# Kernel optimization log

Measured on AMD Instinct MI355X. Metric: run time of the kernel, lower is better.

Reference implementation:

```python
import jax, jax.numpy as jnp
import numpy as np

N_NODES = 50000
N_EDGES = 800000
IN_DIM = 128
HID = 64
HEADS = 4
OUT_DIM = 128
NEG_SLOPE = 0.2


def setup_inputs() -> dict:
    key = jax.random.key(0)
    ks = jax.random.split(key, 11)
    x = jax.random.normal(ks[0], (N_NODES, IN_DIM), dtype=jnp.float32)
    edge_index = jax.random.randint(ks[1], (2, N_EDGES), 0, N_NODES, dtype=jnp.int64)
    s1 = 1.0 / np.sqrt(IN_DIM)
    s2 = 1.0 / np.sqrt(HEADS * HID)
    W1 = jax.random.normal(ks[2], (IN_DIM, HEADS * HID), dtype=jnp.float32) * s1
    a_src1 = jax.random.normal(ks[3], (HEADS, HID), dtype=jnp.float32) * s2
    a_dst1 = jax.random.normal(ks[4], (HEADS, HID), dtype=jnp.float32) * s2
    b1 = jnp.zeros((HEADS * HID,), dtype=jnp.float32)
    W2 = jax.random.normal(ks[5], (HEADS * HID, OUT_DIM), dtype=jnp.float32) * s2
    a_src2 = jax.random.normal(ks[6], (1, OUT_DIM), dtype=jnp.float32) * 0.1
    a_dst2 = jax.random.normal(ks[7], (1, OUT_DIM), dtype=jnp.float32) * 0.1
    b2 = jnp.zeros((OUT_DIM,), dtype=jnp.float32)
    return {"x": x, "edge_index": edge_index, "W1": W1, "a_src1": a_src1,
            "a_dst1": a_dst1, "b1": b1, "W2": W2, "a_src2": a_src2,
            "a_dst2": a_dst2, "b2": b2}


def _gat_conv(x, src, dst, W, a_src, a_dst, bias, heads, out_per_head, concat):
    n = x.shape[0]
    # linear projection per head: [N, H, F]
    h = (x @ W).reshape(n, heads, out_per_head)
    # per-node attention terms: [N, H]
    alpha_src = jnp.einsum('nhf,hf->nh', h, a_src)
    alpha_dst = jnp.einsum('nhf,hf->nh', h, a_dst)
    # edge logits with LeakyReLU: [E, H]
    e = jax.nn.leaky_relu(alpha_src[src] + alpha_dst[dst], NEG_SLOPE)
    # softmax over incoming edges of each destination node
    m = jax.ops.segment_max(e, dst, num_segments=n)  # [N, H]
    m = jnp.where(jnp.isfinite(m), m, 0.0)
    e = jnp.exp(e - m[dst])
    denom = jax.ops.segment_sum(e, dst, num_segments=n)  # [N, H]
    alpha = e / (denom[dst] + 1e-16)  # [E, H]
    # weighted scatter-aggregate of source messages
    out = jax.ops.segment_sum(h[src] * alpha[:, :, None], dst, num_segments=n)  # [N, H, F]
    if concat:
        out = out.reshape(n, heads * out_per_head)
    else:
        out = out.mean(axis=1)
    return out + bias


def reference(x, edge_index, W1, a_src1, a_dst1, b1, W2, a_src2, a_dst2, b2):
    n = x.shape[0]
    # PyG GATConv adds self-loops by default
    loops = jnp.arange(n, dtype=edge_index.dtype)
    src = jnp.concatenate([edge_index[0], loops])
    dst = jnp.concatenate([edge_index[1], loops])
    # dropout layers are identity in inference
    h = _gat_conv(x, src, dst, W1, a_src1, a_dst1, b1, HEADS, HID, True)
    h = jax.nn.elu(h)
    out = _gat_conv(h, src, dst, W2, a_src2, a_dst2, b2, 1, OUT_DIM, True)
    # F.normalize(p=2, dim=1)
    norm = jnp.linalg.norm(out, axis=1, keepdims=True)
    return out / jnp.maximum(norm, 1e-12)
```

## Files before the change

kernel.cpp:

```cpp
#include <hip/hip_runtime.h>
#include <hip/hip_fp16.h>
#include <math.h>

#define N_NODES 50000
#define N_EDGES 800000
#define ET (N_EDGES + N_NODES)
#define IN_DIM 128
#define HID 64
#define HEADS 4
#define C1 (HEADS * HID)
#define OUT_DIM 128
#define NEG_SLOPE 0.2f
#define MTILES 3125
#define G1GRP 782
#define SCAN_B 1024
#define NSCB 49
#define HB 64
#define EPB (N_EDGES / HB)
#define HQ 4
#define NQN (N_NODES / HQ)

typedef _Float16 h8 __attribute__((ext_vector_type(8)));
typedef float f4 __attribute__((ext_vector_type(4)));
typedef unsigned short u16;

__device__ __forceinline__ float leaky(float v) { return fmaxf(v, NEG_SLOPE * v); }
__device__ __forceinline__ float elu(float v) { return v > 0.0f ? v : expm1f(v); }

__device__ __forceinline__ void fma_mix8(float* acc, h8 v, float w) {
    union { h8 h; int i[4]; } u; u.h = v;
#pragma unroll
    for (int k = 0; k < 4; ++k) {
        asm("v_fma_mix_f32 %0, %1, %2, %0 op_sel:[0,0,0] op_sel_hi:[1,0,0]"
            : "+v"(acc[2 * k]) : "v"(u.i[k]), "v"(w));
        asm("v_fma_mix_f32 %0, %1, %2, %0 op_sel:[1,0,0] op_sel_hi:[1,0,0]"
            : "+v"(acc[2 * k + 1]) : "v"(u.i[k]), "v"(w));
    }
}

__global__ void transpose_w(const float* __restrict__ W1, const float* __restrict__ W2,
                            __half* __restrict__ w1t, __half* __restrict__ w2t) {
    int i = blockIdx.x * 256 + threadIdx.x;
    int k1 = i >> 8, n1 = i & 255;
    w1t[n1 * IN_DIM + k1] = __float2half(W1[i]);
    int k2 = i >> 7, n2 = i & 127;
    w2t[n2 * C1 + k2] = __float2half(W2[i]);
}

__global__ __launch_bounds__(256) void gemm1_hist(
        const float* __restrict__ x, const __half* __restrict__ w1t,
        const float* __restrict__ aws, const float* __restrict__ awd,
        __half* __restrict__ hpm, float* __restrict__ as1m, float* __restrict__ ad1m,
        const int* __restrict__ dst, u16* __restrict__ cnt_mat,
        u16* __restrict__ lrank16) {
    __shared__ unsigned pk[NQN / 2];
    if (blockIdx.x < HB) {
        const int b = blockIdx.x, t = threadIdx.x;
        const int e0 = b * EPB;
#pragma unroll
        for (int qd = 0; qd < HQ; ++qd) {
            const int nbase = qd * NQN;
            for (int i = t; i < NQN / 2; i += 256) pk[i] = 0;
            __syncthreads();
            for (int k = t; k < EPB; k += 256) {
                int d = dst[e0 + k] - nbase;
                if ((unsigned)d < (unsigned)NQN) {
                    unsigned r = atomicAdd(&pk[d >> 1], (d & 1) ? 65536u : 1u);
                    lrank16[e0 + k] = (u16)((d & 1) ? (r >> 16) : (r & 0xffffu));
                }
            }
            __syncthreads();
            unsigned* crow = (unsigned*)(cnt_mat + (size_t)b * N_NODES) + qd * (NQN / 2);
            for (int i = t; i < NQN / 2; i += 256) crow[i] = pk[i];
            __syncthreads();
        }
        return;
    }
    const int tile = (blockIdx.x - HB) * 4 + (threadIdx.x >> 6);
    if (tile >= MTILES) return;
    const int lane = threadIdx.x & 63;
    const int m0 = tile * 16, lm = lane & 15, lq = lane >> 4;
    h8 afrag[4];
    const float4* xrow = (const float4*)(x + (size_t)(m0 + lm) * IN_DIM + lq * 8);
#pragma unroll
    for (int kt = 0; kt < 4; ++kt) {
        float4 a = xrow[kt * 8];
        float4 b = xrow[kt * 8 + 1];
        union { h8 v; __half2 p[4]; } u;
        u.p[0] = __floats2half2_rn(a.x, a.y);
        u.p[1] = __floats2half2_rn(a.z, a.w);
        u.p[2] = __floats2half2_rn(b.x, b.y);
        u.p[3] = __floats2half2_rn(b.z, b.w);
        afrag[kt] = u.v;
    }
    f4 acc[16];
#pragma unroll
    for (int nt = 0; nt < 16; ++nt) acc[nt] = (f4){0.f, 0.f, 0.f, 0.f};
#pragma unroll
    for (int nt = 0; nt < 16; ++nt) {
        const h8* brow = (const h8*)(w1t + (size_t)(nt * 16 + lm) * IN_DIM + lq * 8);
#pragma unroll
        for (int kt = 0; kt < 4; ++kt)
            acc[nt] = __builtin_amdgcn_mfma_f32_16x16x32_f16(afrag[kt], brow[kt * 4],
                                                             acc[nt], 0, 0, 0);
    }
    float sS[4][4] = {{0.f}}, sD[4][4] = {{0.f}};
#pragma unroll
    for (int nt = 0; nt < 16; ++nt) {
        int col = nt * 16 + lm;
        float wa = aws[col], wd = awd[col];
        int hd = nt >> 2;
        int pr = nt >> 3;
        int cip = col & 127;
#pragma unroll
        for (int r = 0; r < 4; ++r) {
            float v = acc[nt][r];
            hpm[((size_t)pr * N_NODES + (m0 + lq * 4 + r)) * 128 + cip] = __float2half(v);
            sS[hd][r] += v * wa;
            sD[hd][r] += v * wd;
        }
    }
#pragma unroll
    for (int o = 1; o < 16; o <<= 1) {
#pragma unroll
        for (int hd = 0; hd < 4; ++hd)
#pragma unroll
            for (int r = 0; r < 4; ++r) {
                sS[hd][r] += __shfl_xor(sS[hd][r], o);
                sD[hd][r] += __shfl_xor(sD[hd][r], o);
            }
    }
    if (lm == 0) {
        float2* asp = (float2*)as1m;
        float2* adp = (float2*)ad1m;
#pragma unroll
        for (int r = 0; r < 4; ++r) {
            int row = m0 + lq * 4 + r;
            asp[row]           = make_float2(sS[0][r], sS[1][r]);
            asp[N_NODES + row] = make_float2(sS[2][r], sS[3][r]);
            adp[row]           = make_float2(sD[0][r], sD[1][r]);
            adp[N_NODES + row] = make_float2(sD[2][r], sD[3][r]);
        }
    }
}

__global__ void scan_local(const u16* __restrict__ cnt_mat, u16* __restrict__ boff,
                           int* __restrict__ lscan, int* __restrict__ bsum) {
    __shared__ int wsum[16];
    const int t = threadIdx.x, lane = t & 63, wv = t >> 6;
    int idx = blockIdx.x * SCAN_B + t;
    int run = 0;
    if (idx < N_NODES) {
#pragma unroll 8
        for (int b = 0; b < HB; ++b) {
            u16 c = cnt_mat[(size_t)b * N_NODES + idx];
            boff[(size_t)b * N_NODES + idx] = (u16)run;
            run += c;
        }
    }
    int v = (idx < N_NODES) ? run + 1 : 0;
    int sc = v;
#pragma unroll
    for (int o = 1; o < 64; o <<= 1) {
        int u = __shfl_up(sc, o);
        if (lane >= o) sc += u;
    }
    if (lane == 63) wsum[wv] = sc;
    __syncthreads();
    if (t == 0) {
        int run2 = 0;
#pragma unroll
        for (int w = 0; w < 16; ++w) { int s = wsum[w]; wsum[w] = run2; run2 += s; }
        bsum[blockIdx.x] = run2;
    }
    __syncthreads();
    if (idx < N_NODES) lscan[idx] = sc + wsum[wv];
}

__global__ void scan_final(const int* __restrict__ lscan, const int* __restrict__ bsum,
                           int* __restrict__ rp) {
    __shared__ int base;
    if (threadIdx.x == 0) {
        int s = 0;
        for (int b = 0; b < blockIdx.x; ++b) s += bsum[b];
        base = s;
    }
    __syncthreads();
    int idx = blockIdx.x * SCAN_B + threadIdx.x;
    if (idx == 0) rp[0] = 0;
    if (idx >= N_NODES) return;
    rp[idx + 1] = lscan[idx] + base;
}

__global__ void scatter_plain(const int* __restrict__ src, const int* __restrict__ dst,
                              const u16* __restrict__ lrank16, const u16* __restrict__ boff,
                              const int* __restrict__ rp, u16* __restrict__ cs16) {
    const int tid = blockIdx.x * blockDim.x + threadIdx.x;
    if (tid < N_EDGES / 4) {
        const int b = tid / (EPB / 4);
        const u16* bo = boff + (size_t)b * N_NODES;
        int4 s4 = ((const int4*)src)[tid];
        int4 d4 = ((const int4*)dst)[tid];
        ushort4 r4 = ((const ushort4*)lrank16)[tid];
        cs16[rp[d4.x] + (int)bo[d4.x] + (int)r4.x] = (u16)s4.x;
        cs16[rp[d4.y] + (int)bo[d4.y] + (int)r4.y] = (u16)s4.y;
        cs16[rp[d4.z] + (int)bo[d4.z] + (int)r4.z] = (u16)s4.z;
        cs16[rp[d4.w] + (int)bo[d4.w] + (int)r4.w] = (u16)s4.w;
    } else {
        int d = tid - N_EDGES / 4;
        if (d < N_NODES) cs16[rp[d + 1] - 1] = (u16)d;
    }
}

__global__ __launch_bounds__(256) void gemm2_mfma(
        const __half* __restrict__ ah, const __half* __restrict__ w2t,
        const float* __restrict__ aws, const float* __restrict__ awd,
        __half* __restrict__ h, float* __restrict__ as2, float* __restrict__ ad2) {
    const int tile = blockIdx.x * 4 + (threadIdx.x >> 6);
    if (tile >= MTILES) return;
    const int lane = threadIdx.x & 63;
    const int m0 = tile * 16, lm = lane & 15, lq = lane >> 4;
    h8 afrag[8];
    const h8* arow = (const h8*)(ah + (size_t)(m0 + lm) * C1 + lq * 8);
#pragma unroll
    for (int kt = 0; kt < 8; ++kt) afrag[kt] = arow[kt * 4];
    f4 acc[8];
#pragma unroll
    for (int nt = 0; nt < 8; ++nt) acc[nt] = (f4){0.f, 0.f, 0.f, 0.f};
#pragma unroll
    for (int nt = 0; nt < 8; ++nt) {
        const h8* brow = (const h8*)(w2t + (size_t)(nt * 16 + lm) * C1 + lq * 8);
#pragma unroll
        for (int kt = 0; kt < 8; ++kt)
            acc[nt] = __builtin_amdgcn_mfma_f32_16x16x32_f16(afrag[kt], brow[kt * 4],
                                                             acc[nt], 0, 0, 0);
    }
    float sS[4] = {0.f, 0.f, 0.f, 0.f}, sD[4] = {0.f, 0.f, 0.f, 0.f};
#pragma unroll
    for (int nt = 0; nt < 8; ++nt) {
        int col = nt * 16 + lm;
        float wa = aws[col], wd = awd[col];
#pragma unroll
        for (int r = 0; r < 4; ++r) {
            float v = acc[nt][r];
            h[(size_t)(m0 + lq * 4 + r) * OUT_DIM + col] = __float2half(v);
            sS[r] += v * wa;
            sD[r] += v * wd;
        }
    }
#pragma unroll
    for (int o = 1; o < 16; o <<= 1) {
#pragma unroll
        for (int r = 0; r < 4; ++r) {
            sS[r] += __shfl_xor(sS[r], o);
            sD[r] += __shfl_xor(sD[r], o);
        }
    }
    if (lm == 0) {
#pragma unroll
        for (int r = 0; r < 4; ++r) {
            int row = m0 + lq * 4 + r;
            as2[row] = sS[r];
            ad2[row] = sD[r];
        }
    }
}

__global__ __launch_bounds__(256) void aggregate1_fused(
        const int* __restrict__ rp, const u16* __restrict__ cs16,
        const __half* __restrict__ hpm, const float* __restrict__ as1m,
        const float* __restrict__ ad1m, const float* __restrict__ b1,
        __half* __restrict__ out1h) {
    __shared__ int4 stg[8][32];
    const int pair = blockIdx.x & 1, g = blockIdx.x >> 1;
    const int hw = threadIdx.x >> 5, li = threadIdx.x & 31;
    const int d = g * 8 + hw;
    const int e0 = rp[d], deg = rp[d + 1] - e0;
    const float2* asb = (const float2*)as1m + (size_t)pair * N_NODES;
    const float2 adv = ((const float2*)ad1m)[(size_t)pair * N_NODES + d];
    const char* hb = (const char*)hpm + (size_t)pair * N_NODES * 256;
    const int es = li >> 4, fl = li & 15;
    const int hip = fl >> 3;
    const int lbyte = fl * 16;
    float acc[8] = {0.f, 0.f, 0.f, 0.f, 0.f, 0.f, 0.f, 0.f};
    float ds0 = 0.f, ds1 = 0.f;
    for (int c0 = 0; c0 < deg; c0 += 32) {
        const int clen = min(32, deg - c0);
        int idx = c0 + li;
        bool valid = idx < deg;
        int s = valid ? (int)cs16[e0 + idx] : 0;
        float2 av = asb[s];
        float x0 = valid ? __expf(leaky(av.x + adv.x)) : 0.f;
        float x1 = valid ? __expf(leaky(av.y + adv.y)) : 0.f;
        stg[hw][li] = make_int4(s << 8, __float_as_int(x0), __float_as_int(x1), 0);
        ds0 += x0; ds1 += x1;
        __builtin_amdgcn_wave_barrier();
        int j = 0;
        for (; j + 8 <= clen; j += 8) {
            int4 p0 = stg[hw][j + es];
            int4 p1 = stg[hw][j + 2 + es];
            int4 p2 = stg[hw][j + 4 + es];
            int4 p3 = stg[hw][j + 6 + es];
            h8 v0 = *(const h8*)(hb + p0.x + lbyte);
            h8 v1 = *(const h8*)(hb + p1.x + lbyte);
            h8 v2 = *(const h8*)(hb + p2.x + lbyte);
            h8 v3 = *(const h8*)(hb + p3.x + lbyte);
            fma_mix8(acc, v0, __int_as_float(hip ? p0.z : p0.y));
            fma_mix8(acc, v1, __int_as_float(hip ? p1.z : p1.y));
            fma_mix8(acc, v2, __int_as_float(hip ? p2.z : p2.y));
            fma_mix8(acc, v3, __int_as_float(hip ? p3.z : p3.y));
        }
        for (; j < clen; j += 2) {
            int4 p0 = stg[hw][j + es];
            h8 v0 = *(const h8*)(hb + p0.x + lbyte);
            fma_mix8(acc, v0, __int_as_float(hip ? p0.z : p0.y));
        }
        __builtin_amdgcn_wave_barrier();
    }
#pragma unroll
    for (int f = 0; f < 8; ++f) acc[f] += __shfl_xor(acc[f], 16);
#pragma unroll
    for (int o = 16; o > 0; o >>= 1) {
        ds0 += __shfl_xor(ds0, o);
        ds1 += __shfl_xor(ds1, o);
    }
    if (es == 0) {
        float den = hip ? ds1 : ds0;
        float inv = 1.0f / (den + 1e-16f);
        float4 bA = ((const float4*)b1)[pair * 32 + fl * 2];
        float4 bB = ((const float4*)b1)[pair * 32 + fl * 2 + 1];
        h8 o;
        o[0] = (_Float16)elu(acc[0] * inv + bA.x);
        o[1] = (_Float16)elu(acc[1] * inv + bA.y);
        o[2] = (_Float16)elu(acc[2] * inv + bA.z);
        o[3] = (_Float16)elu(acc[3] * inv + bA.w);
        o[4] = (_Float16)elu(acc[4] * inv + bB.x);
        o[5] = (_Float16)elu(acc[5] * inv + bB.y);
        o[6] = (_Float16)elu(acc[6] * inv + bB.z);
        o[7] = (_Float16)elu(acc[7] * inv + bB.w);
        *(h8*)((char*)out1h + (size_t)d * 512 + pair * 256 + lbyte) = o;
    }
}

__global__ __launch_bounds__(256) void aggregate2_fused(
        const int* __restrict__ rp, const u16* __restrict__ cs16,
        const __half* __restrict__ h2h, const float* __restrict__ as2,
        const float* __restrict__ ad2, const float* __restrict__ b2,
        float* __restrict__ out) {
    __shared__ int2 stg[8][32];
    const int hw = threadIdx.x >> 5, li = threadIdx.x & 31;
    const int d = blockIdx.x * 8 + hw;
    const int e0 = rp[d], deg = rp[d + 1] - e0;
    const float adv = ad2[d];
    const int q = li >> 4, lo = li & 15;
    const int lbyte = lo * 16;
    const char* hbase = (const char*)h2h;
    float acc[8] = {0.f, 0.f, 0.f, 0.f, 0.f, 0.f, 0.f, 0.f};
    float dsum = 0.f;
    for (int c0 = 0; c0 < deg; c0 += 32) {
        const int clen = min(32, deg - c0);
        int idx = c0 + li;
        bool valid = idx < deg;
        int s = valid ? (int)cs16[e0 + idx] : 0;
        float xv = valid ? __expf(leaky(as2[s] + adv)) : 0.f;
        stg[hw][li] = make_int2(s << 8, __float_as_int(xv));
        dsum += xv;
        __builtin_amdgcn_wave_barrier();
        int j = 0;
        for (; j + 8 <= clen; j += 8) {
            int2 p0 = stg[hw][j + q];
            int2 p1 = stg[hw][j + 2 + q];
            int2 p2 = stg[hw][j + 4 + q];
            int2 p3 = stg[hw][j + 6 + q];
            h8 v0 = *(const h8*)(hbase + p0.x + lbyte);
            h8 v1 = *(const h8*)(hbase + p1.x + lbyte);
            h8 v2 = *(const h8*)(hbase + p2.x + lbyte);
            h8 v3 = *(const h8*)(hbase + p3.x + lbyte);
            fma_mix8(acc, v0, __int_as_float(p0.y));
            fma_mix8(acc, v1, __int_as_float(p1.y));
            fma_mix8(acc, v2, __int_as_float(p2.y));
            fma_mix8(acc, v3, __int_as_float(p3.y));
        }
        for (; j < clen; j += 2) {
            int2 p0 = stg[hw][j + q];
            h8 v0 = *(const h8*)(hbase + p0.x + lbyte);
            fma_mix8(acc, v0, __int_as_float(p0.y));
        }
        __builtin_amdgcn_wave_barrier();
    }
#pragma unroll
    for (int f = 0; f < 8; ++f) acc[f] += __shfl_xor(acc[f], 16);
#pragma unroll
    for (int o = 16; o > 0; o >>= 1) dsum += __shfl_xor(dsum, o);
    if (q == 0) {
        float inv = 1.0f / (dsum + 1e-16f);
        float4 bA = ((const float4*)b2)[lo * 2];
        float4 bB = ((const float4*)b2)[lo * 2 + 1];
        float v0 = acc[0] * inv + bA.x, v1 = acc[1] * inv + bA.y;
        float v2 = acc[2] * inv + bA.z, v3 = acc[3] * inv + bA.w;
        float v4 = acc[4] * inv + bB.x, v5 = acc[5] * inv + bB.y;
        float v6 = acc[6] * inv + bB.z, v7 = acc[7] * inv + bB.w;
        float ss = v0 * v0 + v1 * v1 + v2 * v2 + v3 * v3 +
                   v4 * v4 + v5 * v5 + v6 * v6 + v7 * v7;
#pragma unroll
        for (int o = 1; o < 16; o <<= 1) ss += __shfl_xor(ss, o);
        float sc = 1.0f / fmaxf(sqrtf(ss), 1e-12f);
        float4* orow = (float4*)((char*)out + (size_t)d * 512 + lo * 32);
        orow[0] = make_float4(v0 * sc, v1 * sc, v2 * sc, v3 * sc);
        orow[1] = make_float4(v4 * sc, v5 * sc, v6 * sc, v7 * sc);
    }
}

extern "C" void kernel_launch(void* const* d_in, const int* in_sizes, int n_in,
                              void* d_out, int out_size, void* d_ws, size_t ws_size,
                              hipStream_t stream) {
    const float* x     = (const float*)d_in[0];
    const int*   edge  = (const int*)d_in[1];
    const int*   src   = edge;
    const int*   dst   = edge + N_EDGES;
    const float* W1    = (const float*)d_in[2];
    const float* aw_s1 = (const float*)d_in[3];
    const float* aw_d1 = (const float*)d_in[4];
    const float* b1    = (const float*)d_in[5];
    const float* W2    = (const float*)d_in[6];
    const float* aw_s2 = (const float*)d_in[7];
    const float* aw_d2 = (const float*)d_in[8];
    const float* b2    = (const float*)d_in[9];
    float* out = (float*)d_out;

    char* ws = (char*)d_ws;
    size_t off = 0;
    auto alloc = [&](size_t bytes) {
        void* p = ws + off;
        off += (bytes + 255) & ~(size_t)255;
        return p;
    };
    u16*    cs16    = (u16*)alloc((size_t)ET * 2);
    u16*    lrank16 = (u16*)alloc((size_t)N_EDGES * 2);
    u16*    cnt_mat = (u16*)alloc((size_t)HB * N_NODES * 2);
    u16*    boff    = (u16*)alloc((size_t)HB * N_NODES * 2);
    int*    rp      = (int*)alloc((size_t)(N_NODES + 1) * 4);
    int*    lscan   = (int*)alloc((size_t)NSCB * SCAN_B * 4);
    int*    bsum    = (int*)alloc((size_t)NSCB * 4);
    float*  as1     = (float*)alloc((size_t)N_NODES * HEADS * 4);
    float*  ad1     = (float*)alloc((size_t)N_NODES * HEADS * 4);
    float*  as2     = (float*)alloc((size_t)N_NODES * 4);
    float*  ad2     = (float*)alloc((size_t)N_NODES * 4);
    __half* w1t     = (__half*)alloc((size_t)IN_DIM * C1 * 2);
    __half* w2t     = (__half*)alloc((size_t)C1 * OUT_DIM * 2);
    __half* hpm     = (__half*)alloc((size_t)N_NODES * C1 * 2);
    __half* out1h   = (__half*)alloc((size_t)N_NODES * C1 * 2);
    __half* h2h     = hpm;
    (void)off;


    transpose_w<<<(IN_DIM * C1) / 256, 256, 0, stream>>>(W1, W2, w1t, w2t);

    gemm1_hist<<<HB + G1GRP, 256, 0, stream>>>(x, w1t, aw_s1, aw_d1, hpm, as1, ad1,
                                               dst, cnt_mat, lrank16);

    scan_local<<<NSCB, SCAN_B, 0, stream>>>(cnt_mat, boff, lscan, bsum);
    scan_final<<<NSCB, SCAN_B, 0, stream>>>(lscan, bsum, rp);
    scatter_plain<<<(N_EDGES / 4 + N_NODES + 255) / 256, 256, 0, stream>>>(
        src, dst, lrank16, boff, rp, cs16);

    aggregate1_fused<<<(N_NODES / 8) * 2, 256, 0, stream>>>(rp, cs16, hpm, as1, ad1, b1, out1h);

    gemm2_mfma<<<(MTILES + 3) / 4, 256, 0, stream>>>(out1h, w2t, aw_s2, aw_d2, h2h, as2, ad2);
    aggregate2_fused<<<N_NODES / 8, 256, 0, stream>>>(rp, cs16, h2h, as2, ad2, b2, out);
}
```

Before: 306.3 us.

## Split fused gemm1/histogram kernel into separate hist and GEMM launches

Splits the kernel that co-scheduled the edge histogram with the first projection GEMM into a standalone histogram kernel and a standalone MFMA GEMM launched after the scatter. The histogram now uses two node halves with a larger 50KB shared array instead of four quarters, and reads dst as int4 vectors. The intent is to stop the large LDS allocation from limiting occupancy of the GEMM blocks and to cut histogram passes. The cost is an extra launch and no more overlap between histogram and GEMM, and the 64 histogram blocks run on their own with little parallelism.

```diff
diff --git a/kernel.cpp b/kernel.cpp
--- a/kernel.cpp
+++ b/kernel.cpp
@@ -12,13 +12,10 @@
 #define OUT_DIM 128
 #define NEG_SLOPE 0.2f
 #define MTILES 3125
-#define G1GRP 782
 #define SCAN_B 1024
 #define NSCB 49
 #define HB 64
 #define EPB (N_EDGES / HB)
-#define HQ 4
-#define NQN (N_NODES / HQ)
 
 typedef _Float16 h8 __attribute__((ext_vector_type(8)));
 typedef float f4 __attribute__((ext_vector_type(4)));
@@ -47,100 +44,43 @@
     w2t[n2 * C1 + k2] = __float2half(W2[i]);
 }
 
-__global__ __launch_bounds__(256) void gemm1_hist(
-        const float* __restrict__ x, const __half* __restrict__ w1t,
-        const float* __restrict__ aws, const float* __restrict__ awd,
-        __half* __restrict__ hpm, float* __restrict__ as1m, float* __restrict__ ad1m,
+__global__ __launch_bounds__(256) void hist_kernel(
         const int* __restrict__ dst, u16* __restrict__ cnt_mat,
         u16* __restrict__ lrank16) {
-    __shared__ unsigned pk[NQN / 2];
-    if (blockIdx.x < HB) {
-        const int b = blockIdx.x, t = threadIdx.x;
-        const int e0 = b * EPB;
-#pragma unroll
-        for (int qd = 0; qd < HQ; ++qd) {
-            const int nbase = qd * NQN;
-            for (int i = t; i < NQN / 2; i += 256) pk[i] = 0;
-            __syncthreads();
-            for (int k = t; k < EPB; k += 256) {
-                int d = dst[e0 + k] - nbase;
-                if ((unsigned)d < (unsigned)NQN) {
-                    unsigned r = atomicAdd(&pk[d >> 1], (d & 1) ? 65536u : 1u);
-                    lrank16[e0 + k] = (u16)((d & 1) ? (r >> 16) : (r & 0xffffu));
-                }
+    __shared__ unsigned pk[N_NODES / 4];
+    const int b = blockIdx.x, t = threadIdx.x;
+    const int e0 = b * EPB;
+    const int4* d4p = (const int4*)(dst + e0);
+#pragma unroll
+    for (int half = 0; half < 2; ++half) {
+        const int nbase = half * (N_NODES / 2);
+        for (int i = t; i < N_NODES / 4; i += 256) pk[i] = 0;
+        __syncthreads();
+        for (int k4 = t; k4 < EPB / 4; k4 += 256) {
+            int4 d4 = d4p[k4];
+            int dd0 = d4.x - nbase, dd1 = d4.y - nbase;
+            int dd2 = d4.z - nbase, dd3 = d4.w - nbase;
+            if ((unsigned)dd0 < (unsigned)(N_NODES / 2)) {
+                unsigned r = atomicAdd(&pk[dd0 >> 1], (dd0 & 1) ? 65536u : 1u);
+                lrank16[e0 + k4 * 4 + 0] = (u16)((dd0 & 1) ? (r >> 16) : (r & 0xffffu));
             }
-            __syncthreads();
-            unsigned* crow = (unsigned*)(cnt_mat + (size_t)b * N_NODES) + qd * (NQN / 2);
-            for (int i = t; i < NQN / 2; i += 256) crow[i] = pk[i];
-            __syncthreads();
-        }
-        return;
-    }
-    const int tile = (blockIdx.x - HB) * 4 + (threadIdx.x >> 6);
-    if (tile >= MTILES) return;
-    const int lane = threadIdx.x & 63;
-    const int m0 = tile * 16, lm = lane & 15, lq = lane >> 4;
-    h8 afrag[4];
-    const float4* xrow = (const float4*)(x + (size_t)(m0 + lm) * IN_DIM + lq * 8);
-#pragma unroll
-    for (int kt = 0; kt < 4; ++kt) {
-        float4 a = xrow[kt * 8];
-        float4 b = xrow[kt * 8 + 1];
-        union { h8 v; __half2 p[4]; } u;
-        u.p[0] = __floats2half2_rn(a.x, a.y);
-        u.p[1] = __floats2half2_rn(a.z, a.w);
-        u.p[2] = __floats2half2_rn(b.x, b.y);
-        u.p[3] = __floats2half2_rn(b.z, b.w);
-        afrag[kt] = u.v;
-    }
-    f4 acc[16];
-#pragma unroll
-    for (int nt = 0; nt < 16; ++nt) acc[nt] = (f4){0.f, 0.f, 0.f, 0.f};
-#pragma unroll
-    for (int nt = 0; nt < 16; ++nt) {
-        const h8* brow = (const h8*)(w1t + (size_t)(nt * 16 + lm) * IN_DIM + lq * 8);
-#pragma unroll
-        for (int kt = 0; kt < 4; ++kt)
-            acc[nt] = __builtin_amdgcn_mfma_f32_16x16x32_f16(afrag[kt], brow[kt * 4],
-                                                             acc[nt], 0, 0, 0);
-    }
-    float sS[4][4] = {{0.f}}, sD[4][4] = {{0.f}};
-#pragma unroll
-    for (int nt = 0; nt < 16; ++nt) {
-        int col = nt * 16 + lm;
-        float wa = aws[col], wd = awd[col];
-        int hd = nt >> 2;
-        int pr = nt >> 3;
-        int cip = col & 127;
-#pragma unroll
-        for (int r = 0; r < 4; ++r) {
-            float v = acc[nt][r];
-            hpm[((size_t)pr * N_NODES + (m0 + lq * 4 + r)) * 128 + cip] = __float2half(v);
-            sS[hd][r] += v * wa;
-            sD[hd][r] += v * wd;
-        }
-    }
-#pragma unroll
-    for (int o = 1; o < 16; o <<= 1) {
-#pragma unroll
-        for (int hd = 0; hd < 4; ++hd)
-#pragma unroll
-            for (int r = 0; r < 4; ++r) {
-                sS[hd][r] += __shfl_xor(sS[hd][r], o);
-                sD[hd][r] += __shfl_xor(sD[hd][r], o);
+            if ((unsigned)dd1 < (unsigned)(N_NODES / 2)) {
+                unsigned r = atomicAdd(&pk[dd1 >> 1], (dd1 & 1) ? 65536u : 1u);
+                lrank16[e0 + k4 * 4 + 1] = (u16)((dd1 & 1) ? (r >> 16) : (r & 0xffffu));
             }
-    }
-    if (lm == 0) {
-        float2* asp = (float2*)as1m;
-        float2* adp = (float2*)ad1m;
-#pragma unroll
-        for (int r = 0; r < 4; ++r) {
-            int row = m0 + lq * 4 + r;
-            asp[row]           = make_float2(sS[0][r], sS[1][r]);
-            asp[N_NODES + row] = make_float2(sS[2][r], sS[3][r]);
-            adp[row]           = make_float2(sD[0][r], sD[1][r]);
-            adp[N_NODES + row] = make_float2(sD[2][r], sD[3][r]);
-        }
+            if ((unsigned)dd2 < (unsigned)(N_NODES / 2)) {
+                unsigned r = atomicAdd(&pk[dd2 >> 1], (dd2 & 1) ? 65536u : 1u);
+                lrank16[e0 + k4 * 4 + 2] = (u16)((dd2 & 1) ? (r >> 16) : (r & 0xffffu));
+            }
+            if ((unsigned)dd3 < (unsigned)(N_NODES / 2)) {
+                unsigned r = atomicAdd(&pk[dd3 >> 1], (dd3 & 1) ? 65536u : 1u);
+                lrank16[e0 + k4 * 4 + 3] = (u16)((dd3 & 1) ? (r >> 16) : (r & 0xffffu));
+            }
+        }
+        __syncthreads();
+        unsigned* crow = (unsigned*)(cnt_mat + (size_t)b * N_NODES) + half * (N_NODES / 4);
+        for (int i = t; i < N_NODES / 4; i += 256) crow[i] = pk[i];
+        __syncthreads();
     }
 }
 
@@ -209,6 +149,78 @@
     } else {
         int d = tid - N_EDGES / 4;
         if (d < N_NODES) cs16[rp[d + 1] - 1] = (u16)d;
+    }
+}
+
+__global__ __launch_bounds__(256) void gemm1_mfma(
+        const float* __restrict__ x, const __half* __restrict__ w1t,
+        const float* __restrict__ aws, const float* __restrict__ awd,
+        __half* __restrict__ hpm, float* __restrict__ as1m, float* __restrict__ ad1m) {
+    const int tile = blockIdx.x * 4 + (threadIdx.x >> 6);
+    if (tile >= MTILES) return;
+    const int lane = threadIdx.x & 63;
+    const int m0 = tile * 16, lm = lane & 15, lq = lane >> 4;
+    h8 afrag[4];
+    const float4* xrow = (const float4*)(x + (size_t)(m0 + lm) * IN_DIM + lq * 8);
+#pragma unroll
+    for (int kt = 0; kt < 4; ++kt) {
+        float4 a = xrow[kt * 8];
+        float4 b = xrow[kt * 8 + 1];
+        union { h8 v; __half2 p[4]; } u;
+        u.p[0] = __floats2half2_rn(a.x, a.y);
+        u.p[1] = __floats2half2_rn(a.z, a.w);
+        u.p[2] = __floats2half2_rn(b.x, b.y);
+        u.p[3] = __floats2half2_rn(b.z, b.w);
+        afrag[kt] = u.v;
+    }
+    f4 acc[16];
+#pragma unroll
+    for (int nt = 0; nt < 16; ++nt) acc[nt] = (f4){0.f, 0.f, 0.f, 0.f};
+#pragma unroll
+    for (int nt = 0; nt < 16; ++nt) {
+        const h8* brow = (const h8*)(w1t + (size_t)(nt * 16 + lm) * IN_DIM + lq * 8);
+#pragma unroll
+        for (int kt = 0; kt < 4; ++kt)
+            acc[nt] = __builtin_amdgcn_mfma_f32_16x16x32_f16(afrag[kt], brow[kt * 4],
+                                                             acc[nt], 0, 0, 0);
+    }
+    float sS[4][4] = {{0.f}}, sD[4][4] = {{0.f}};
+#pragma unroll
+    for (int nt = 0; nt < 16; ++nt) {
+        int col = nt * 16 + lm;
+        float wa = aws[col], wd = awd[col];
+        int hd = nt >> 2;
+        int pr = nt >> 3;
+        int cip = col & 127;
+#pragma unroll
+        for (int r = 0; r < 4; ++r) {
+            float v = acc[nt][r];
+            hpm[((size_t)pr * N_NODES + (m0 + lq * 4 + r)) * 128 + cip] = __float2half(v);
+            sS[hd][r] += v * wa;
+            sD[hd][r] += v * wd;
+        }
+    }
+#pragma unroll
+    for (int o = 1; o < 16; o <<= 1) {
+#pragma unroll
+        for (int hd = 0; hd < 4; ++hd)
+#pragma unroll
+            for (int r = 0; r < 4; ++r) {
+                sS[hd][r] += __shfl_xor(sS[hd][r], o);
+                sD[hd][r] += __shfl_xor(sD[hd][r], o);
+            }
+    }
+    if (lm == 0) {
+        float2* asp = (float2*)as1m;
+        float2* adp = (float2*)ad1m;
+#pragma unroll
+        for (int r = 0; r < 4; ++r) {
+            int row = m0 + lq * 4 + r;
+            asp[row]           = make_float2(sS[0][r], sS[1][r]);
+            asp[N_NODES + row] = make_float2(sS[2][r], sS[3][r]);
+            adp[row]           = make_float2(sD[0][r], sD[1][r]);
+            adp[N_NODES + row] = make_float2(sD[2][r], sD[3][r]);
+        }
     }
 }
 
@@ -455,15 +467,13 @@
 
 
     transpose_w<<<(IN_DIM * C1) / 256, 256, 0, stream>>>(W1, W2, w1t, w2t);
-
-    gemm1_hist<<<HB + G1GRP, 256, 0, stream>>>(x, w1t, aw_s1, aw_d1, hpm, as1, ad1,
-                                               dst, cnt_mat, lrank16);
-
+    hist_kernel<<<HB, 256, 0, stream>>>(dst, cnt_mat, lrank16);
     scan_local<<<NSCB, SCAN_B, 0, stream>>>(cnt_mat, boff, lscan, bsum);
     scan_final<<<NSCB, SCAN_B, 0, stream>>>(lscan, bsum, rp);
     scatter_plain<<<(N_EDGES / 4 + N_NODES + 255) / 256, 256, 0, stream>>>(
         src, dst, lrank16, boff, rp, cs16);
 
+    gemm1_mfma<<<(MTILES + 3) / 4, 256, 0, stream>>>(x, w1t, aw_s1, aw_d1, hpm, as1, ad1);
     aggregate1_fused<<<(N_NODES / 8) * 2, 256, 0, stream>>>(rp, cs16, hpm, as1, ad1, b1, out1h);
 
     gemm2_mfma<<<(MTILES + 3) / 4, 256, 0, stream>>>(out1h, w2t, aw_s2, aw_d2, h2h, as2, ad2);
```

Measured after the change: 302.5 us. About the same (-1.2%).
